# Performance work log

Hardware: AMD Instinct MI355X
Metric: run time of the kernel (lower is better)

## Reference

```python
import jax, jax.numpy as jnp
import numpy as np

N_NODES = 4096
N_EDGES = 32768
PE_DIM = 16
HIDDEN = 128


def setup_inputs() -> dict:
    key = jax.random.key(0)
    k_nodes, k_send, k_recv, k_w = jax.random.split(key, 4)
    nodes = jax.random.normal(k_nodes, (N_NODES, 8), dtype=jnp.float32)
    senders = jax.random.randint(k_send, (N_EDGES,), 0, N_NODES)
    receivers = jax.random.randint(k_recv, (N_EDGES,), 0, N_NODES)
    W = jax.random.normal(k_w, (PE_DIM, HIDDEN), dtype=jnp.float32) / np.sqrt(PE_DIM).astype(np.float32)
    b = jnp.zeros((HIDDEN,), dtype=jnp.float32)
    return {"nodes": nodes, "senders": senders, "receivers": receivers, "W": W, "b": b}


def reference(nodes, senders, receivers, W, b):
    n = nodes.shape[0]
    pe_dim = W.shape[0]
    # out-degree per node (clamped at 1, as in the original)
    ones = jnp.ones(senders.shape[0], dtype=jnp.float32)
    degree = jnp.maximum(jax.ops.segment_sum(ones, senders, num_segments=n), 1.0)
    inv_deg_e = (1.0 / degree)[senders]  # [E], per-edge 1/deg(sender)

    prob = jnp.eye(n, dtype=jnp.float32)  # [n, n] landing probabilities
    diags = []
    for _ in range(pe_dim):
        # gather sender rows, normalize, scatter-add into receiver rows
        msg = prob[senders] * inv_deg_e[:, None]           # [E, n]
        prob = jax.ops.segment_sum(msg, receivers, num_segments=n)  # [n, n]
        diags.append(jnp.diagonal(prob))                    # return probability A^k_ii
    pe = jnp.stack(diags, axis=-1)  # [n, pe_dim]
    return pe @ W + b               # [n, hidden]
```

## Files before the change

### kernel.cpp

```cpp
#include <hip/hip_runtime.h>

#define NN 4096
#define NE 32768
#define PED 16
#define HID 128
#define CW 16
#define NCHUNK 64
#define THREADS 1024
#define PASSES 4

typedef _Float16 h_t;
typedef _Float16 h8 __attribute__((ext_vector_type(8)));
typedef unsigned long long u64;

__device__ __forceinline__ int xp(int p) {
  int g = ((p & 3) << 1) | ((p >> 2) & 1);
  return ((p >> 2) << 7) | (g << 4);
}


__global__ void count_kernel(const int* __restrict__ senders,
                             const int* __restrict__ receivers,
                             int* __restrict__ outdeg, int* __restrict__ indeg) {
  int e = blockIdx.x * blockDim.x + threadIdx.x;
  if (e < NE) {
    atomicAdd(&outdeg[senders[e]], 1);
    atomicAdd(&indeg[receivers[e]], 1);
  }
}

__global__ void sort_kernel(const int* __restrict__ indeg, const int* __restrict__ outdeg,
                            float* __restrict__ dinv,
                            int* __restrict__ rowperm, int* __restrict__ sortpos,
                            int* __restrict__ chunk_off, int* __restrict__ chunk_len) {
  __shared__ int hist[64];
  __shared__ int base[64];
  int t = threadIdx.x;
  if (t < 64) hist[t] = 0;
  __syncthreads();
  for (int r = t; r < NN; r += 256) {
    int d = indeg[r]; if (d > 63) d = 63;
    atomicAdd(&hist[d], 1);
    int od = outdeg[r]; if (od < 1) od = 1;
    dinv[r] = 1.0f / (float)od;
  }
  __syncthreads();
  if (t == 0) {
    int acc = 0;
    for (int i = 0; i < 64; ++i) { base[i] = acc; acc += hist[i]; }
  }
  __syncthreads();
  for (int r = t; r < NN; r += 256) {
    int d = indeg[r]; if (d > 63) d = 63;
    int pos = atomicAdd(&base[d], 1);
    rowperm[pos] = r;
    sortpos[r] = pos;
  }
  __syncthreads();
  if (t < NCHUNK) {
    int m = 0;
    for (int i = 0; i < 64; ++i) {
      int d = indeg[rowperm[(t << 6) + i]];
      if (d > m) m = d;
    }
    chunk_len[t] = (m + 1) & ~1;
  }
  __syncthreads();
  if (t == 0) {
    int acc = 0;
    for (int c = 0; c < NCHUNK; ++c) { chunk_off[c] = acc; acc += chunk_len[c] << 6; }
    chunk_off[NCHUNK] = acc;
  }
}

__global__ void zero_tail(const int* __restrict__ chunk_off, int2* __restrict__ e2) {
  int total = chunk_off[NCHUNK];
  e2[total + threadIdx.x] = make_int2(0, 0);
}

__global__ void fill_ell(const int* __restrict__ senders, const int* __restrict__ receivers,
                         const int* __restrict__ sortpos, const int* __restrict__ chunk_off,
                         const float* __restrict__ dinv, int* __restrict__ fillc,
                         int2* __restrict__ ell) {
  int e = blockIdx.x * blockDim.x + threadIdx.x;
  if (e < NE) {
    int r = receivers[e], s = senders[e];
    int p = sortpos[r];
    int tslot = atomicAdd(&fillc[r], 1);
    int slot = chunk_off[p >> 6] + (tslot << 6) + (p & 63);
    ell[slot] = make_int2(xp(sortpos[s]), __float_as_int(dinv[s]));
  }
}

__global__ void sched_ell(const int* __restrict__ chunk_off,
                          const int* __restrict__ chunk_len,
                          const int* __restrict__ rowperm,
                          const int* __restrict__ indeg,
                          const int2* __restrict__ src, int2* __restrict__ dst) {
  int tid = blockIdx.x * blockDim.x + threadIdx.x;
  if (tid >= NCHUNK * 8) return;
  int c = tid >> 3;
  int trk = tid & 7;
  int base = chunk_off[c];
  int len = chunk_len[c];
  int l0 = trk << 3;

  int d[8];
  u64 freeL[8];
  int dmax = 0;
#pragma unroll
  for (int j = 0; j < 8; ++j) {
    int dd = indeg[rowperm[(c << 6) + l0 + j]];
    if (dd > 63) dd = 63;
    d[j] = dd;
    if (dd > dmax) dmax = dd;
  }
  if (len > 63) {
#pragma unroll
    for (int j = 0; j < 8; ++j) {
      for (int t = 0; t < d[j]; ++t) dst[base + (t << 6) + l0 + j] = src[base + (t << 6) + l0 + j];
      for (int t = d[j]; t < len; ++t) dst[base + (t << 6) + l0 + j] = make_int2(((t + j) & 7) << 4, 0);
    }
    return;
  }
  u64 full = (len == 0) ? 0 : ((1ull << len) - 1);
#pragma unroll
  for (int j = 0; j < 8; ++j) freeL[j] = full;
  u64 fC[8];
#pragma unroll
  for (int q = 0; q < 8; ++q) fC[q] = full;

  for (int t = 0; t < dmax; ++t) {
#pragma unroll
    for (int j = 0; j < 8; ++j) {
      if (t < d[j]) {
        int2 e = src[base + (t << 6) + l0 + j];
        int cls = (e.x >> 4) & 7;
        u64 fc = 0;
#pragma unroll
        for (int q = 0; q < 8; ++q) fc = (q == cls) ? fC[q] : fc;
        u64 avail = freeL[j] & fc;
        u64 pool = avail ? avail : freeL[j];
        u64 pick = pool & (~pool + 1);
        int slab = __builtin_ctzll(pick);
        freeL[j] &= ~pick;
        if (avail) {
#pragma unroll
          for (int q = 0; q < 8; ++q) if (q == cls) fC[q] &= ~pick;
        }
        dst[base + (slab << 6) + l0 + j] = e;
      }
    }
  }
#pragma unroll
  for (int j = 0; j < 8; ++j) {
    u64 rem = freeL[j];
    while (rem) {
      u64 pick = rem & (~rem + 1);
      rem &= rem - 1;
      int slab = __builtin_ctzll(pick);
      int cls = 0;
#pragma unroll
      for (int q = 7; q >= 0; --q) if (fC[q] & pick) cls = q;
#pragma unroll
      for (int q = 0; q < 8; ++q) if (q == cls) fC[q] &= ~pick;
      dst[base + (slab << 6) + l0 + j] = make_int2(cls << 4, 0);
    }
  }
}


#define MIXL(acc, srcv) \
  asm("v_fma_mix_f32 %0, %1, %2, %0 op_sel_hi:[1,0,0]" : "+v"(acc) : "v"(srcv), "v"(w))
#define MIXH(acc, srcv) \
  asm("v_fma_mix_f32 %0, %1, %2, %0 op_sel:[1,0,0] op_sel_hi:[1,0,0]" : "+v"(acc) : "v"(srcv), "v"(w))

#define MIX16(lo, hi) \
  MIXL(a[0], lo.x);  MIXH(a[1], lo.x);  \
  MIXL(a[2], lo.y);  MIXH(a[3], lo.y);  \
  MIXL(a[4], lo.z);  MIXH(a[5], lo.z);  \
  MIXL(a[6], lo.w);  MIXH(a[7], lo.w);  \
  MIXL(a[8], hi.x);  MIXH(a[9], hi.x);  \
  MIXL(a[10], hi.y); MIXH(a[11], hi.y); \
  MIXL(a[12], hi.z); MIXH(a[13], hi.z); \
  MIXL(a[14], hi.w); MIXH(a[15], hi.w)

__global__ __launch_bounds__(THREADS, 4)
void fused_kernel(const int2* __restrict__ ell,
                  const int* __restrict__ chunk_off,
                  const int* __restrict__ chunk_len,
                  const int* __restrict__ rowperm,
                  float* __restrict__ pe) {
  __shared__ __align__(16) h_t X[NN * CW];
  char* Xb = (char*)X;
  int c0 = blockIdx.x * CW;
  int tid = threadIdx.x;
  int wave = tid >> 6, lane = tid & 63;

  for (int p = tid; p < NN; p += THREADS) {
    int dd = rowperm[p] - c0;
    h8 lo8, hi8;
#pragma unroll
    for (int j = 0; j < 8; ++j) {
      lo8[j] = (h_t)((dd == j) ? 1.0f : 0.0f);
      hi8[j] = (h_t)((dd == 8 + j) ? 1.0f : 0.0f);
    }
    int xb = xp(p);
    *reinterpret_cast<h8*>(Xb + xb) = lo8;
    *reinterpret_cast<h8*>(Xb + (xb ^ 16)) = hi8;
  }
  __syncthreads();

  for (int k = 0; k < PED; ++k) {
    h8 rlo[PASSES], rhi[PASSES];
#pragma unroll
    for (int pass = 0; pass < PASSES; ++pass) {
      int chunk = (pass << 4) + ((pass & 1) ? (15 - wave) : wave);
      int base = chunk_off[chunk];
      int len = chunk_len[chunk];
      int r = rowperm[(chunk << 6) + lane];
      float a[16];
#pragma unroll
      for (int j = 0; j < 16; ++j) a[j] = 0.f;
      const int2* ep = ell + base + lane;
      int2 e0 = ep[0];
      int2 e1 = ep[64];
      int2 e2 = ep[128];
      int2 e3 = ep[192];
      int4 lo0 = *reinterpret_cast<const int4*>(Xb + e0.x);
      int4 hi0 = *reinterpret_cast<const int4*>(Xb + (e0.x ^ 16));
      for (int t = 0; t < len; t += 2) {
        int2 e4 = ep[256], e5 = ep[320];
        ep += 128;
        int4 lo1 = *reinterpret_cast<const int4*>(Xb + e1.x);
        int4 hi1 = *reinterpret_cast<const int4*>(Xb + (e1.x ^ 16));
        float w = __int_as_float(e0.y);
        MIX16(lo0, hi0);
        int4 nlo = *reinterpret_cast<const int4*>(Xb + e2.x);
        int4 nhi = *reinterpret_cast<const int4*>(Xb + (e2.x ^ 16));
        w = __int_as_float(e1.y);
        MIX16(lo1, hi1);
        e0 = e2; e1 = e3; e2 = e4; e3 = e5;
        lo0 = nlo; hi0 = nhi;
      }
      h8 plo, phi;
#pragma unroll
      for (int j = 0; j < 8; ++j) { plo[j] = (h_t)a[j]; phi[j] = (h_t)a[8 + j]; }
      rlo[pass] = plo; rhi[pass] = phi;
      int dj = r - c0;
      if (dj >= 0 && dj < CW) {
        float dv = a[0];
#pragma unroll
        for (int j = 1; j < 16; ++j) dv = (dj == j) ? a[j] : dv;
        pe[r * PED + k] = dv;
      }
    }
    __syncthreads();
#pragma unroll
    for (int pass = 0; pass < PASSES; ++pass) {
      int chunk = (pass << 4) + ((pass & 1) ? (15 - wave) : wave);
      int xb = xp((chunk << 6) + lane);
      *reinterpret_cast<h8*>(Xb + xb) = rlo[pass];
      *reinterpret_cast<h8*>(Xb + (xb ^ 16)) = rhi[pass];
    }
    __syncthreads();
  }
}

__global__ void out_kernel(const float* __restrict__ pe, const float* __restrict__ W,
                           const float* __restrict__ bvec, float* __restrict__ out) {
  __shared__ float sW[PED * HID];
  int r = blockIdx.x;
  int h = threadIdx.x;
  for (int i = h; i < PED * HID; i += HID) sW[i] = W[i];
  __syncthreads();
  float acc = bvec[h];
  float p[PED];
#pragma unroll
  for (int kk = 0; kk < PED; ++kk) p[kk] = pe[r * PED + kk];
#pragma unroll
  for (int kk = 0; kk < PED; ++kk) acc = fmaf(p[kk], sW[kk * HID + h], acc);
  out[r * HID + h] = acc;
}

extern "C" void kernel_launch(void* const* d_in, const int* in_sizes, int n_in,
                              void* d_out, int out_size, void* d_ws, size_t ws_size,
                              hipStream_t stream) {
  const int* senders = (const int*)d_in[1];
  const int* receivers = (const int*)d_in[2];
  const float* W = (const float*)d_in[3];
  const float* bvec = (const float*)d_in[4];
  float* out = (float*)d_out;

  char* p = (char*)d_ws;
  int* outdeg = (int*)p;    p += (size_t)NN * 4;
  int* indeg = (int*)p;     p += (size_t)NN * 4;
  int* fillc = (int*)p;     p += (size_t)NN * 4;
  float* dinv = (float*)p;  p += (size_t)NN * 4;
  int* rowperm = (int*)p;   p += (size_t)NN * 4;
  int* sortpos = (int*)p;   p += (size_t)NN * 4;
  int* chunk_off = (int*)p; p += 128 * 4;
  int* chunk_len = (int*)p; p += 128 * 4;
  float* pe = (float*)p;    p += (size_t)NN * PED * 4;
  size_t ell_slots = (size_t)64 * NE + 1024;
  int2* ell = (int2*)p;     p += ell_slots * sizeof(int2);
  int2* ell2 = (int2*)p;

  hipMemsetAsync(d_ws, 0, (size_t)NN * 4 * 3, stream);
  count_kernel<<<NE / 256, 256, 0, stream>>>(senders, receivers, outdeg, indeg);
  sort_kernel<<<1, 256, 0, stream>>>(indeg, outdeg, dinv, rowperm, sortpos, chunk_off, chunk_len);
  zero_tail<<<1, 512, 0, stream>>>(chunk_off, ell2);
  fill_ell<<<NE / 256, 256, 0, stream>>>(senders, receivers, sortpos, chunk_off, dinv, fillc, ell);
  sched_ell<<<2, 256, 0, stream>>>(chunk_off, chunk_len, rowperm, indeg, ell, ell2);

  fused_kernel<<<NN / CW, THREADS, 0, stream>>>(ell2, chunk_off, chunk_len, rowperm, pe);

  out_kernel<<<NN, HID, 0, stream>>>(pe, W, bvec, out);
}
```

Measured before the change: 246.1 us.

## Deepen software pipeline in fused SpMM loop and prefetch ELL entries in scheduler

The main gather-accumulate loop moves from a two-deep prefetch to a four-deep pipeline: it keeps eight ELL entries and four LDS row pairs in flight, unrolls by four, and handles a two-edge tail. This is meant to hide LDS and global load latency behind the FMA-mix work. The scheduling kernel now prefetches the next slab of entries into registers, and its launch shape changes from 2x256 to 8x64 threads. The padded tail buffer and the zero_tail launch are enlarged to cover the deeper lookahead reads, at the cost of more register pressure in a kernel capped by its launch bounds.

```diff
diff --git a/kernel.cpp b/kernel.cpp
--- a/kernel.cpp
+++ b/kernel.cpp
@@ -130,11 +130,16 @@
 #pragma unroll
   for (int q = 0; q < 8; ++q) fC[q] = full;
 
+  int2 cur[8], nxt[8];
+#pragma unroll
+  for (int j = 0; j < 8; ++j) cur[j] = src[base + l0 + j];
   for (int t = 0; t < dmax; ++t) {
+#pragma unroll
+    for (int j = 0; j < 8; ++j) nxt[j] = src[base + ((t + 1) << 6) + l0 + j];
 #pragma unroll
     for (int j = 0; j < 8; ++j) {
       if (t < d[j]) {
-        int2 e = src[base + (t << 6) + l0 + j];
+        int2 e = cur[j];
         int cls = (e.x >> 4) & 7;
         u64 fc = 0;
 #pragma unroll
@@ -151,6 +156,8 @@
         dst[base + (slab << 6) + l0 + j] = e;
       }
     }
+#pragma unroll
+    for (int j = 0; j < 8; ++j) cur[j] = nxt[j];
   }
 #pragma unroll
   for (int j = 0; j < 8; ++j) {
@@ -184,6 +191,8 @@
   MIXL(a[10], hi.y); MIXH(a[11], hi.y); \
   MIXL(a[12], hi.z); MIXH(a[13], hi.z); \
   MIXL(a[14], hi.w); MIXH(a[15], hi.w)
+
+#define LDSR(dst, addr) dst = *reinterpret_cast<const int4*>(Xb + (addr))
 
 __global__ __launch_bounds__(THREADS, 4)
 void fused_kernel(const int2* __restrict__ ell,
@@ -222,27 +231,34 @@
       float a[16];
 #pragma unroll
       for (int j = 0; j < 16; ++j) a[j] = 0.f;
+
       const int2* ep = ell + base + lane;
-      int2 e0 = ep[0];
-      int2 e1 = ep[64];
-      int2 e2 = ep[128];
-      int2 e3 = ep[192];
-      int4 lo0 = *reinterpret_cast<const int4*>(Xb + e0.x);
-      int4 hi0 = *reinterpret_cast<const int4*>(Xb + (e0.x ^ 16));
-      for (int t = 0; t < len; t += 2) {
-        int2 e4 = ep[256], e5 = ep[320];
-        ep += 128;
-        int4 lo1 = *reinterpret_cast<const int4*>(Xb + e1.x);
-        int4 hi1 = *reinterpret_cast<const int4*>(Xb + (e1.x ^ 16));
-        float w = __int_as_float(e0.y);
-        MIX16(lo0, hi0);
-        int4 nlo = *reinterpret_cast<const int4*>(Xb + e2.x);
-        int4 nhi = *reinterpret_cast<const int4*>(Xb + (e2.x ^ 16));
-        w = __int_as_float(e1.y);
-        MIX16(lo1, hi1);
-        e0 = e2; e1 = e3; e2 = e4; e3 = e5;
-        lo0 = nlo; hi0 = nhi;
+      int2 e[8];
+#pragma unroll
+      for (int i = 0; i < 8; ++i) e[i] = ep[i << 6];
+      int4 xl[4], xh[4];
+#pragma unroll
+      for (int i = 0; i < 4; ++i) { LDSR(xl[i], e[i].x); LDSR(xh[i], e[i].x ^ 16); }
+      int t = 0;
+      for (; t + 4 <= len; t += 4) {
+        ep += 256;
+#pragma unroll
+        for (int i = 0; i < 4; ++i) {
+          float w = __int_as_float(e[i].y);
+          MIX16(xl[i], xh[i]);
+          LDSR(xl[i], e[i + 4].x);
+          LDSR(xh[i], e[i + 4].x ^ 16);
+          e[i] = e[i + 4];
+          e[i + 4] = ep[(i + 4) << 6];
+        }
       }
+      if (t < len) {
+        float w = __int_as_float(e[0].y);
+        MIX16(xl[0], xh[0]);
+        w = __int_as_float(e[1].y);
+        MIX16(xl[1], xh[1]);
+      }
+
       h8 plo, phi;
 #pragma unroll
       for (int j = 0; j < 8; ++j) { plo[j] = (h_t)a[j]; phi[j] = (h_t)a[8 + j]; }
@@ -302,16 +318,16 @@
   int* chunk_off = (int*)p; p += 128 * 4;
   int* chunk_len = (int*)p; p += 128 * 4;
   float* pe = (float*)p;    p += (size_t)NN * PED * 4;
-  size_t ell_slots = (size_t)64 * NE + 1024;
+  size_t ell_slots = (size_t)64 * NE + 2048;
   int2* ell = (int2*)p;     p += ell_slots * sizeof(int2);
   int2* ell2 = (int2*)p;
 
   hipMemsetAsync(d_ws, 0, (size_t)NN * 4 * 3, stream);
   count_kernel<<<NE / 256, 256, 0, stream>>>(senders, receivers, outdeg, indeg);
   sort_kernel<<<1, 256, 0, stream>>>(indeg, outdeg, dinv, rowperm, sortpos, chunk_off, chunk_len);
-  zero_tail<<<1, 512, 0, stream>>>(chunk_off, ell2);
+  zero_tail<<<1, 1024, 0, stream>>>(chunk_off, ell2);
   fill_ell<<<NE / 256, 256, 0, stream>>>(senders, receivers, sortpos, chunk_off, dinv, fillc, ell);
-  sched_ell<<<2, 256, 0, stream>>>(chunk_off, chunk_len, rowperm, indeg, ell, ell2);
+  sched_ell<<<8, 64, 0, stream>>>(chunk_off, chunk_len, rowperm, indeg, ell, ell2);
 
   fused_kernel<<<NN / CW, THREADS, 0, stream>>>(ell2, chunk_off, chunk_len, rowperm, pe);
 
```

New measurement: 248.7 us. About the same (+1.1%).

## Merge degree counting and sort into one block, trim preprocessing launches

Applied to the files above, without the earlier changes.

Degree counting moves into a single 1024-thread block that uses shared-memory atomics and also sorts, which removes the memset, the count kernel and the zero_tail kernel. The tail zeroing moves into sched_ell, which now prefetches the next ELL row into registers and launches as 8 blocks of 64 threads. The fused kernel hoists its per-pass chunk metadata and row lookups out of the k loop. The aim is to cut launch count and serial preprocessing latency, at the risk that one block doing 32K atomics becomes a serial bottleneck.

```diff
diff --git a/kernel.cpp b/kernel.cpp
--- a/kernel.cpp
+++ b/kernel.cpp
@@ -19,40 +19,41 @@
 }
 
 
-__global__ void count_kernel(const int* __restrict__ senders,
-                             const int* __restrict__ receivers,
-                             int* __restrict__ outdeg, int* __restrict__ indeg) {
-  int e = blockIdx.x * blockDim.x + threadIdx.x;
-  if (e < NE) {
-    atomicAdd(&outdeg[senders[e]], 1);
-    atomicAdd(&indeg[receivers[e]], 1);
-  }
-}
-
-__global__ void sort_kernel(const int* __restrict__ indeg, const int* __restrict__ outdeg,
-                            float* __restrict__ dinv,
-                            int* __restrict__ rowperm, int* __restrict__ sortpos,
-                            int* __restrict__ chunk_off, int* __restrict__ chunk_len) {
+__global__ void sort_all(const int* __restrict__ senders, const int* __restrict__ receivers,
+                         float* __restrict__ dinv, int* __restrict__ indeg_g,
+                         int* __restrict__ fillc,
+                         int* __restrict__ rowperm, int* __restrict__ sortpos,
+                         int* __restrict__ chunk_off, int* __restrict__ chunk_len) {
+  __shared__ int ld_in[NN];
+  __shared__ int ld_out[NN];
   __shared__ int hist[64];
-  __shared__ int base[64];
+  __shared__ int hbase[64];
   int t = threadIdx.x;
+  for (int i = t; i < NN; i += 1024) { ld_in[i] = 0; ld_out[i] = 0; }
   if (t < 64) hist[t] = 0;
   __syncthreads();
-  for (int r = t; r < NN; r += 256) {
-    int d = indeg[r]; if (d > 63) d = 63;
+  for (int e = t; e < NE; e += 1024) {
+    atomicAdd(&ld_out[senders[e]], 1);
+    atomicAdd(&ld_in[receivers[e]], 1);
+  }
+  __syncthreads();
+  for (int r = t; r < NN; r += 1024) {
+    int od = ld_out[r]; if (od < 1) od = 1;
+    dinv[r] = 1.0f / (float)od;
+    fillc[r] = 0;
+    int d = ld_in[r]; if (d > 63) d = 63;
+    indeg_g[r] = d;
     atomicAdd(&hist[d], 1);
-    int od = outdeg[r]; if (od < 1) od = 1;
-    dinv[r] = 1.0f / (float)od;
   }
   __syncthreads();
   if (t == 0) {
     int acc = 0;
-    for (int i = 0; i < 64; ++i) { base[i] = acc; acc += hist[i]; }
-  }
-  __syncthreads();
-  for (int r = t; r < NN; r += 256) {
-    int d = indeg[r]; if (d > 63) d = 63;
-    int pos = atomicAdd(&base[d], 1);
+    for (int i = 0; i < 64; ++i) { hbase[i] = acc; acc += hist[i]; }
+  }
+  __syncthreads();
+  for (int r = t; r < NN; r += 1024) {
+    int d = ld_in[r]; if (d > 63) d = 63;
+    int pos = atomicAdd(&hbase[d], 1);
     rowperm[pos] = r;
     sortpos[r] = pos;
   }
@@ -60,7 +61,8 @@
   if (t < NCHUNK) {
     int m = 0;
     for (int i = 0; i < 64; ++i) {
-      int d = indeg[rowperm[(t << 6) + i]];
+      int rr = rowperm[(t << 6) + i];
+      int d = ld_in[rr]; if (d > 63) d = 63;
       if (d > m) m = d;
     }
     chunk_len[t] = (m + 1) & ~1;
@@ -71,11 +73,6 @@
     for (int c = 0; c < NCHUNK; ++c) { chunk_off[c] = acc; acc += chunk_len[c] << 6; }
     chunk_off[NCHUNK] = acc;
   }
-}
-
-__global__ void zero_tail(const int* __restrict__ chunk_off, int2* __restrict__ e2) {
-  int total = chunk_off[NCHUNK];
-  e2[total + threadIdx.x] = make_int2(0, 0);
 }
 
 __global__ void fill_ell(const int* __restrict__ senders, const int* __restrict__ receivers,
@@ -99,6 +96,10 @@
                           const int2* __restrict__ src, int2* __restrict__ dst) {
   int tid = blockIdx.x * blockDim.x + threadIdx.x;
   if (tid >= NCHUNK * 8) return;
+  {
+    int total = chunk_off[NCHUNK];
+    for (int i = tid; i < 2048; i += 512) dst[total + i] = make_int2(0, 0);
+  }
   int c = tid >> 3;
   int trk = tid & 7;
   int base = chunk_off[c];
@@ -111,7 +112,6 @@
 #pragma unroll
   for (int j = 0; j < 8; ++j) {
     int dd = indeg[rowperm[(c << 6) + l0 + j]];
-    if (dd > 63) dd = 63;
     d[j] = dd;
     if (dd > dmax) dmax = dd;
   }
@@ -130,11 +130,16 @@
 #pragma unroll
   for (int q = 0; q < 8; ++q) fC[q] = full;
 
+  int2 cur[8], nxt[8];
+#pragma unroll
+  for (int j = 0; j < 8; ++j) cur[j] = src[base + l0 + j];
   for (int t = 0; t < dmax; ++t) {
+#pragma unroll
+    for (int j = 0; j < 8; ++j) nxt[j] = src[base + ((t + 1) << 6) + l0 + j];
 #pragma unroll
     for (int j = 0; j < 8; ++j) {
       if (t < d[j]) {
-        int2 e = src[base + (t << 6) + l0 + j];
+        int2 e = cur[j];
         int cls = (e.x >> 4) & 7;
         u64 fc = 0;
 #pragma unroll
@@ -151,6 +156,8 @@
         dst[base + (slab << 6) + l0 + j] = e;
       }
     }
+#pragma unroll
+    for (int j = 0; j < 8; ++j) cur[j] = nxt[j];
   }
 #pragma unroll
   for (int j = 0; j < 8; ++j) {
@@ -197,6 +204,18 @@
   int tid = threadIdx.x;
   int wave = tid >> 6, lane = tid & 63;
 
+  int baseB[PASSES], lenB[PASSES], rB[PASSES], djB[PASSES], xbW[PASSES];
+#pragma unroll
+  for (int pass = 0; pass < PASSES; ++pass) {
+    int chunk = (pass << 4) + ((pass & 1) ? (15 - wave) : wave);
+    baseB[pass] = chunk_off[chunk];
+    lenB[pass] = chunk_len[chunk];
+    int rr = rowperm[(chunk << 6) + lane];
+    rB[pass] = rr;
+    djB[pass] = rr - c0;
+    xbW[pass] = xp((chunk << 6) + lane);
+  }
+
   for (int p = tid; p < NN; p += THREADS) {
     int dd = rowperm[p] - c0;
     h8 lo8, hi8;
@@ -215,10 +234,8 @@
     h8 rlo[PASSES], rhi[PASSES];
 #pragma unroll
     for (int pass = 0; pass < PASSES; ++pass) {
-      int chunk = (pass << 4) + ((pass & 1) ? (15 - wave) : wave);
-      int base = chunk_off[chunk];
-      int len = chunk_len[chunk];
-      int r = rowperm[(chunk << 6) + lane];
+      int base = baseB[pass];
+      int len = lenB[pass];
       float a[16];
 #pragma unroll
       for (int j = 0; j < 16; ++j) a[j] = 0.f;
@@ -247,19 +264,18 @@
 #pragma unroll
       for (int j = 0; j < 8; ++j) { plo[j] = (h_t)a[j]; phi[j] = (h_t)a[8 + j]; }
       rlo[pass] = plo; rhi[pass] = phi;
-      int dj = r - c0;
+      int dj = djB[pass];
       if (dj >= 0 && dj < CW) {
         float dv = a[0];
 #pragma unroll
         for (int j = 1; j < 16; ++j) dv = (dj == j) ? a[j] : dv;
-        pe[r * PED + k] = dv;
+        pe[rB[pass] * PED + k] = dv;
       }
     }
     __syncthreads();
 #pragma unroll
     for (int pass = 0; pass < PASSES; ++pass) {
-      int chunk = (pass << 4) + ((pass & 1) ? (15 - wave) : wave);
-      int xb = xp((chunk << 6) + lane);
+      int xb = xbW[pass];
       *reinterpret_cast<h8*>(Xb + xb) = rlo[pass];
       *reinterpret_cast<h8*>(Xb + (xb ^ 16)) = rhi[pass];
     }
@@ -293,7 +309,6 @@
   float* out = (float*)d_out;
 
   char* p = (char*)d_ws;
-  int* outdeg = (int*)p;    p += (size_t)NN * 4;
   int* indeg = (int*)p;     p += (size_t)NN * 4;
   int* fillc = (int*)p;     p += (size_t)NN * 4;
   float* dinv = (float*)p;  p += (size_t)NN * 4;
@@ -302,16 +317,14 @@
   int* chunk_off = (int*)p; p += 128 * 4;
   int* chunk_len = (int*)p; p += 128 * 4;
   float* pe = (float*)p;    p += (size_t)NN * PED * 4;
-  size_t ell_slots = (size_t)64 * NE + 1024;
+  size_t ell_slots = (size_t)64 * NE + 2048;
   int2* ell = (int2*)p;     p += ell_slots * sizeof(int2);
   int2* ell2 = (int2*)p;
 
-  hipMemsetAsync(d_ws, 0, (size_t)NN * 4 * 3, stream);
-  count_kernel<<<NE / 256, 256, 0, stream>>>(senders, receivers, outdeg, indeg);
-  sort_kernel<<<1, 256, 0, stream>>>(indeg, outdeg, dinv, rowperm, sortpos, chunk_off, chunk_len);
-  zero_tail<<<1, 512, 0, stream>>>(chunk_off, ell2);
+  sort_all<<<1, 1024, 0, stream>>>(senders, receivers, dinv, indeg, fillc,
+                                   rowperm, sortpos, chunk_off, chunk_len);
   fill_ell<<<NE / 256, 256, 0, stream>>>(senders, receivers, sortpos, chunk_off, dinv, fillc, ell);
-  sched_ell<<<2, 256, 0, stream>>>(chunk_off, chunk_len, rowperm, indeg, ell, ell2);
+  sched_ell<<<8, 64, 0, stream>>>(chunk_off, chunk_len, rowperm, indeg, ell, ell2);
 
   fused_kernel<<<NN / CW, THREADS, 0, stream>>>(ell2, chunk_off, chunk_len, rowperm, pe);
 
```

After: 208.1 us. 15.4% less time.
